# Kernel tuning notes

Hardware: AMD Instinct MI355X
Metric: run time of the kernel (lower is better)

## Reference

```python
import jax, jax.numpy as jnp
import numpy as np

N = 50000
E = 800000
F_IN = 128
HEADS = 4
OUT_PER_HEAD = 32  # out_features 128 / 4 heads
NEG_SLOPE = 0.2


def setup_inputs() -> dict:
    key = jax.random.key(0)
    k1, k2, k3, k4, k5 = jax.random.split(key, 5)
    x = jax.random.normal(k1, (N, F_IN), dtype=jnp.float32)
    edge_index = jax.random.randint(k2, (2, E), 0, N, dtype=jnp.int64)
    # xavier-uniform style init
    limW = float(np.sqrt(6.0 / (F_IN + OUT_PER_HEAD)))
    W = jax.random.uniform(k3, (HEADS, F_IN, OUT_PER_HEAD), jnp.float32, -limW, limW)
    lima = float(np.sqrt(6.0 / (OUT_PER_HEAD + 1)))
    a_l = jax.random.uniform(k4, (HEADS, OUT_PER_HEAD), jnp.float32, -lima, lima)
    a_r = jax.random.uniform(k5, (HEADS, OUT_PER_HEAD), jnp.float32, -lima, lima)
    return {"x": x, "edge_index": edge_index, "W": W, "a_l": a_l, "a_r": a_r}


def _leaky_relu(v, slope):
    return jnp.where(v >= 0, v, slope * v)


def reference(x, edge_index, W, a_l, a_r):
    src, dst = edge_index[0], edge_index[1]
    n = x.shape[0]
    # Wh: [heads, N, out_per_head]
    Wh = jnp.einsum('nf,kfh->knh', x, W)
    e_l = jnp.einsum('knh,kh->kn', Wh, a_l)  # [heads, N]
    e_r = jnp.einsum('knh,kh->kn', Wh, a_r)
    # per-edge attention logits [heads, E]
    e = _leaky_relu(e_l[:, src] + e_r[:, dst], NEG_SLOPE)
    # segment softmax over incoming edges of each dst node
    seg_max = jax.vmap(lambda ee: jax.ops.segment_max(ee, dst, num_segments=n))(e)
    seg_max = jnp.maximum(seg_max, -1e9)  # torch init value for empty nodes
    exp_e = jnp.exp(e - seg_max[:, dst])
    denom = jax.vmap(lambda ee: jax.ops.segment_sum(ee, dst, num_segments=n))(exp_e)
    alpha = exp_e / (denom[:, dst] + 1e-16)  # [heads, E]
    # weighted aggregation: [heads, E, out_per_head] scattered into [heads, N, out_per_head]
    weighted = alpha[..., None] * Wh[:, src, :]
    out = jax.vmap(lambda w: jax.ops.segment_sum(w, dst, num_segments=n))(weighted)
    # concat heads -> [N, heads*out_per_head]
    return out.transpose(1, 0, 2).reshape(n, -1)
```

## Files before the change

kernel.cpp:

```cpp
#include <hip/hip_runtime.h>

#define NN 50000
#define NE 800000
#define FIN 128
#define NH 4
#define OPH 32
#define FOUT 128
#define NSLOPE 0.2f
#define NGB ((NN + 63) / 64)
#define BCOLS 144
#define LDA 136
#define BSH 5
#define BUKSZ 32
#define NBUK ((NN + BUKSZ - 1) >> BSH)
#define SUBCH 4096
#define NPSUB ((NE + SUBCH - 1) / SUBCH)
#define NSC ((NPSUB + 3) / 4)
#define SLOTQ 15
#define SLOTS 64
#define GRID1 (NPSUB + NGB)

typedef __attribute__((ext_vector_type(8))) short short8v;
typedef __attribute__((ext_vector_type(4))) float f32x4;

static __device__ __forceinline__ unsigned short f2bf(float f) {
  unsigned int u = __float_as_uint(f);
  u += 0x7fffu + ((u >> 16) & 1u);
  return (unsigned short)(u >> 16);
}

__global__ __launch_bounds__(128) void k_prep(
    const float* __restrict__ W, const float* __restrict__ a_l,
    const float* __restrict__ a_r, unsigned short* __restrict__ Btf) {
  const int c = blockIdx.x;
  const int f = threadIdx.x;
  unsigned short v = 0;
  if (c < 128) {
    const int h = c >> 5, o = c & 31;
    v = f2bf(W[h * (FIN * OPH) + f * OPH + o]);
  } else if (c < 136) {
    const int j = c - 128;
    const int h = j & 3;
    const float* __restrict__ av = (j < 4) ? a_l : a_r;
    float s = 0.f;
    for (int o = 0; o < 32; ++o)
      s += W[h * (FIN * OPH) + f * OPH + o] * av[h * OPH + o];
    v = f2bf(s);
  }
  const int ct = c >> 4, lr = c & 15;
  const int s = f >> 5, rem = f & 31, lk = rem >> 3, j = rem & 7;
  const int l = lr + 16 * lk;
  Btf[(((size_t)ct * 4 + s) * 64 + l) * 8 + j] = v;
}

__global__ __launch_bounds__(256) void k_gemm_part(
    const float* __restrict__ x, const unsigned short* __restrict__ Btf,
    const int* __restrict__ src, const int* __restrict__ dst,
    unsigned int* __restrict__ ebuf,
    unsigned short* __restrict__ WhU, float* __restrict__ e_l4,
    float* __restrict__ e_r4) {
  __shared__ union U {
    unsigned short As[64 * LDA];
    int cntl[NBUK];
  } sh;
  const int t = threadIdx.x;
  const int bid = blockIdx.x;

  if (bid < NPSUB) {
    const int pidx = bid;
    const int sc = pidx >> 2;
    const int sub = pidx & 3;
    const int base = pidx * SUBCH;
    for (int b = t; b < NBUK; b += 256) sh.cntl[b] = 0;
    __syncthreads();
    unsigned int* __restrict__ myreg =
        ebuf + (size_t)sc * NBUK * 64 + sub * 16;
#pragma unroll
    for (int k = 0; k < SUBCH / 256; ++k) {
      const int i = base + k * 256 + t;
      if (i < NE) {
        const int d = dst[i];
        const int b = d >> BSH;
        const int lp = atomicAdd(&sh.cntl[b], 1);
        if (lp < SLOTQ)
          myreg[(size_t)b * 64 + 1 + lp] =
              ((unsigned int)(d & (BUKSZ - 1)) << 16) | (unsigned int)src[i];
      }
    }
    __syncthreads();
    for (int b = t; b < NBUK; b += 256)
      myreg[(size_t)b * 64] = (unsigned int)min(sh.cntl[b], SLOTQ);
    return;
  }

  const int g = bid - NPSUB;
  if (g >= NGB) return;
  const int m0 = g * 64;

#pragma unroll
  for (int i = 0; i < 8; ++i) {
    const int fidx = t + i * 256;
    const int node = fidx >> 5;
    const int fg = fidx & 31;
    const int n = m0 + node;
    float4 v = make_float4(0.f, 0.f, 0.f, 0.f);
    if (n < NN) v = *(const float4*)(x + (size_t)n * FIN + fg * 4);
    ushort4 pk;
    pk.x = f2bf(v.x); pk.y = f2bf(v.y); pk.z = f2bf(v.z); pk.w = f2bf(v.w);
    *(ushort4*)&sh.As[node * LDA + fg * 4] = pk;
  }
  __syncthreads();

  const int w = t >> 6;
  const int l = t & 63;
  const int lr = l & 15;
  const int lk = l >> 4;

  short8v a_frag[4];
#pragma unroll
  for (int kk = 0; kk < 4; ++kk)
    a_frag[kk] = *(const short8v*)&sh.As[(w * 16 + lr) * LDA + kk * 32 + lk * 8];

  f32x4 acc[9];
#pragma unroll
  for (int ct = 0; ct < 9; ++ct) acc[ct] = (f32x4){0.f, 0.f, 0.f, 0.f};

#pragma unroll
  for (int ct = 0; ct < 9; ++ct) {
    const unsigned short* __restrict__ Bp = Btf + ((size_t)ct * 4) * 512 + l * 8;
    short8v b0 = *(const short8v*)(Bp);
    short8v b1 = *(const short8v*)(Bp + 512);
    short8v b2 = *(const short8v*)(Bp + 1024);
    short8v b3 = *(const short8v*)(Bp + 1536);
    acc[ct] = __builtin_amdgcn_mfma_f32_16x16x32_bf16(a_frag[0], b0, acc[ct], 0, 0, 0);
    acc[ct] = __builtin_amdgcn_mfma_f32_16x16x32_bf16(a_frag[1], b1, acc[ct], 0, 0, 0);
    acc[ct] = __builtin_amdgcn_mfma_f32_16x16x32_bf16(a_frag[2], b2, acc[ct], 0, 0, 0);
    acc[ct] = __builtin_amdgcn_mfma_f32_16x16x32_bf16(a_frag[3], b3, acc[ct], 0, 0, 0);
  }

#pragma unroll
  for (int ct = 0; ct < 9; ++ct) {
#pragma unroll
    for (int reg = 0; reg < 4; ++reg) {
      const int n = m0 + w * 16 + lk * 4 + reg;
      if (n >= NN) continue;
      const float v = acc[ct][reg];
      if (ct < 8) {
        WhU[(size_t)n * FOUT + ct * 16 + lr] = f2bf(v);
      } else if (lr < 4) {
        e_l4[n * NH + lr] = v;
      } else if (lr < 8) {
        e_r4[n * NH + (lr - 4)] = v;
      }
    }
  }
}

__global__ __launch_bounds__(256) void k_lists(
    const unsigned int* __restrict__ ebuf,
    unsigned short* __restrict__ lists_g, int* __restrict__ degs) {
  __shared__ __align__(16) unsigned short lists[BUKSZ][SLOTS];
  __shared__ int cur[BUKSZ];

  const int b = blockIdx.x;
  const int t = threadIdx.x;
  const int w = t >> 6;
  const int lane = t & 63;

  if (t < BUKSZ) cur[t] = 0;
  __syncthreads();

  const int word = lane & 15;
#pragma unroll
  for (int it = 0; it < (NPSUB + 15) / 16; ++it) {
    const int j = it * 16 + w * 4 + (lane >> 4);
    unsigned int v = 0;
    if (j < NPSUB) {
      const int sc = j >> 2, sub = j & 3;
      v = ebuf[(size_t)sc * NBUK * 64 + (size_t)b * 64 + sub * 16 + word];
    }
    const unsigned int cnt = __shfl(v, lane & 48);
    if (j < NPSUB && word >= 1 && word <= (int)cnt) {
      const int idx = (int)(v >> 16);
      const int lp = atomicAdd(&cur[idx], 1);
      if (lp < SLOTS) lists[idx][lp] = (unsigned short)(v & 0xFFFFu);
    }
  }
  __syncthreads();

  const int idx = t >> 3, ch = t & 7;
  const int node = b * BUKSZ + idx;
  if (node < NN) {
    const uint4 pk = *(const uint4*)&lists[idx][ch * 8];
    *(uint4*)&lists_g[(size_t)node * SLOTS + ch * 8] = pk;
  }
  if (t < BUKSZ && b * BUKSZ + t < NN)
    degs[b * BUKSZ + t] = min(cur[t], SLOTS);
}

__global__ __launch_bounds__(256) void k_agg(
    const int* __restrict__ degs, const unsigned short* __restrict__ lists_g,
    const float* __restrict__ e_l4, const float* __restrict__ e_r4,
    const unsigned int* __restrict__ Whh, float* __restrict__ out) {
  __shared__ unsigned short ls[4][64];
  __shared__ float exs[4][64][4];

  const int t = threadIdx.x;
  const int w = t >> 6;
  const int lane = t & 63;
  const int n = blockIdx.x * 4 + w;

  const int deg = min(degs[n], SLOTS);
  const float4 ern = *(const float4*)&e_r4[n * NH];
  const unsigned short s16 = lists_g[(size_t)n * SLOTS + lane];
  ls[w][lane] = s16;

  float e0 = 0.f, e1 = 0.f, e2 = 0.f, e3 = 0.f;
  if (lane < deg) {
    const int s = (int)s16;
    const float4 el = *(const float4*)&e_l4[s * NH];
    float l0 = el.x + ern.x; l0 = (l0 >= 0.f) ? l0 : NSLOPE * l0;
    float l1 = el.y + ern.y; l1 = (l1 >= 0.f) ? l1 : NSLOPE * l1;
    float l2 = el.z + ern.z; l2 = (l2 >= 0.f) ? l2 : NSLOPE * l2;
    float l3 = el.w + ern.w; l3 = (l3 >= 0.f) ? l3 : NSLOPE * l3;
    e0 = __expf(l0); e1 = __expf(l1);
    e2 = __expf(l2); e3 = __expf(l3);
  }
  *(float4*)exs[w][lane] = make_float4(e0, e1, e2, e3);

  const int h = lane >> 4;
  float acc0 = 0.f, acc1 = 0.f, den = 0.f;
  int jl = 0;
  for (; jl + 7 < deg; jl += 8) {
    int sj[8];
#pragma unroll
    for (int u = 0; u < 8; ++u) sj[u] = ls[w][jl + u];
    unsigned int vv[8];
#pragma unroll
    for (int u = 0; u < 8; ++u) vv[u] = Whh[(size_t)sj[u] * 64 + lane];
#pragma unroll
    for (int u = 0; u < 8; ++u) {
      const float wH = exs[w][jl + u][h];
      den += wH;
      acc0 = fmaf(wH, __uint_as_float(vv[u] << 16), acc0);
      acc1 = fmaf(wH, __uint_as_float(vv[u] & 0xffff0000u), acc1);
    }
  }
  for (; jl < deg; ++jl) {
    const int sj = ls[w][jl];
    const float wH = exs[w][jl][h];
    const unsigned int v = Whh[(size_t)sj * 64 + lane];
    den += wH;
    acc0 = fmaf(wH, __uint_as_float(v << 16), acc0);
    acc1 = fmaf(wH, __uint_as_float(v & 0xffff0000u), acc1);
  }

  const float inv = 1.f / (den + 1e-16f);
  *(float2*)&out[(size_t)n * FOUT + 2 * lane] =
      make_float2(acc0 * inv, acc1 * inv);
}

extern "C" void kernel_launch(void* const* d_in, const int* in_sizes, int n_in,
                              void* d_out, int out_size, void* d_ws, size_t ws_size,
                              hipStream_t stream) {
  const float* x   = (const float*)d_in[0];
  const int*   ei  = (const int*)d_in[1];
  const float* W   = (const float*)d_in[2];
  const float* a_l = (const float*)d_in[3];
  const float* a_r = (const float*)d_in[4];
  float* out = (float*)d_out;

  const int* src = ei;
  const int* dst = ei + NE;

  unsigned int* Whh = (unsigned int*)d_ws;
  float* e_l4     = (float*)(Whh + (size_t)NN * 64);
  float* e_r4     = e_l4 + NN * NH;
  unsigned short* Btf = (unsigned short*)(e_r4 + NN * NH);
  unsigned int* ebuf = (unsigned int*)(Btf + 9 * 4 * 64 * 8);
  unsigned short* lists_g = (unsigned short*)(ebuf + (size_t)NSC * NBUK * 64);
  int* degs = (int*)(lists_g + (size_t)NN * SLOTS);
  (void)ws_size; (void)in_sizes; (void)n_in; (void)out_size;

  k_prep<<<BCOLS, 128, 0, stream>>>(W, a_l, a_r, Btf);

  k_gemm_part<<<GRID1, 256, 0, stream>>>(
      x, Btf, src, dst, ebuf, (unsigned short*)Whh, e_l4, e_r4);

  k_lists<<<NBUK, 256, 0, stream>>>(ebuf, lists_g, degs);

  k_agg<<<NN / 4, 256, 0, stream>>>(degs, lists_g, e_l4, e_r4, Whh, out);
}
```

Measured before the change: 70.28 us.

## Split Wh into per-head planes and aggregate one head per block

The GEMM now writes Wh as four head-major bf16 planes of shape [N,32] instead of one interleaved [N,128] row. The aggregation kernel launches one block per (head, 4-node group) and swizzles block IDs so neighbouring blocks share a head, which shrinks each gather's working set to one head's plane and is meant to improve L2 reuse. Each wave splits the edges across two half-waves, gathering 2-byte values per lane, and combines the halves with a shuffle. The cost is four times as many blocks, redundant reads of degrees and lists per head, and narrower 16-bit gathers. The lists kernel also zero-fills its shared slots so unused entries no longer hold stale data.

```diff
diff --git a/kernel.cpp b/kernel.cpp
--- a/kernel.cpp
+++ b/kernel.cpp
@@ -57,7 +57,7 @@
     const float* __restrict__ x, const unsigned short* __restrict__ Btf,
     const int* __restrict__ src, const int* __restrict__ dst,
     unsigned int* __restrict__ ebuf,
-    unsigned short* __restrict__ WhU, float* __restrict__ e_l4,
+    unsigned short* __restrict__ WhhH, float* __restrict__ e_l4,
     float* __restrict__ e_r4) {
   __shared__ union U {
     unsigned short As[64 * LDA];
@@ -146,7 +146,8 @@
       if (n >= NN) continue;
       const float v = acc[ct][reg];
       if (ct < 8) {
-        WhU[(size_t)n * FOUT + ct * 16 + lr] = f2bf(v);
+        const int h2 = ct >> 1;
+        WhhH[((size_t)h2 * NN + n) * 32 + (ct & 1) * 16 + lr] = f2bf(v);
       } else if (lr < 4) {
         e_l4[n * NH + lr] = v;
       } else if (lr < 8) {
@@ -168,6 +169,11 @@
   const int lane = t & 63;
 
   if (t < BUKSZ) cur[t] = 0;
+  {
+    const int idx0 = t >> 3, ch0 = t & 7;
+    uint4 z; z.x = z.y = z.z = z.w = 0u;
+    *(uint4*)&lists[idx0][ch0 * 8] = z;
+  }
   __syncthreads();
 
   const int word = lane & 15;
@@ -201,63 +207,70 @@
 __global__ __launch_bounds__(256) void k_agg(
     const int* __restrict__ degs, const unsigned short* __restrict__ lists_g,
     const float* __restrict__ e_l4, const float* __restrict__ e_r4,
-    const unsigned int* __restrict__ Whh, float* __restrict__ out) {
+    const unsigned short* __restrict__ WhhH, float* __restrict__ out) {
   __shared__ unsigned short ls[4][64];
-  __shared__ float exs[4][64][4];
+  __shared__ float exs[4][64];
 
   const int t = threadIdx.x;
   const int w = t >> 6;
   const int lane = t & 63;
-  const int n = blockIdx.x * 4 + w;
+  const int bid = blockIdx.x;
+
+  const int h = (bid & 7) >> 1;
+  const int ng = (bid >> 3) * 2 + (bid & 1);
+  const int n = ng * 4 + w;
 
   const int deg = min(degs[n], SLOTS);
-  const float4 ern = *(const float4*)&e_r4[n * NH];
+  const float ern = e_r4[n * NH + h];
   const unsigned short s16 = lists_g[(size_t)n * SLOTS + lane];
-  ls[w][lane] = s16;
-
-  float e0 = 0.f, e1 = 0.f, e2 = 0.f, e3 = 0.f;
+  ls[w][lane] = (lane < deg) ? s16 : (unsigned short)0;
+
+  float e = 0.f;
   if (lane < deg) {
-    const int s = (int)s16;
-    const float4 el = *(const float4*)&e_l4[s * NH];
-    float l0 = el.x + ern.x; l0 = (l0 >= 0.f) ? l0 : NSLOPE * l0;
-    float l1 = el.y + ern.y; l1 = (l1 >= 0.f) ? l1 : NSLOPE * l1;
-    float l2 = el.z + ern.z; l2 = (l2 >= 0.f) ? l2 : NSLOPE * l2;
-    float l3 = el.w + ern.w; l3 = (l3 >= 0.f) ? l3 : NSLOPE * l3;
-    e0 = __expf(l0); e1 = __expf(l1);
-    e2 = __expf(l2); e3 = __expf(l3);
-  }
-  *(float4*)exs[w][lane] = make_float4(e0, e1, e2, e3);
-
-  const int h = lane >> 4;
-  float acc0 = 0.f, acc1 = 0.f, den = 0.f;
+    float l = e_l4[(int)s16 * NH + h] + ern;
+    l = (l >= 0.f) ? l : NSLOPE * l;
+    e = __expf(l);
+  }
+  exs[w][lane] = e;
+
+  const int col = lane & 31;
+  const int eh = lane >> 5;
+  const unsigned short* __restrict__ T = WhhH + (size_t)h * NN * 32;
+
+  float acc = 0.f, den = 0.f;
   int jl = 0;
   for (; jl + 7 < deg; jl += 8) {
-    int sj[8];
-#pragma unroll
-    for (int u = 0; u < 8; ++u) sj[u] = ls[w][jl + u];
-    unsigned int vv[8];
-#pragma unroll
-    for (int u = 0; u < 8; ++u) vv[u] = Whh[(size_t)sj[u] * 64 + lane];
-#pragma unroll
-    for (int u = 0; u < 8; ++u) {
-      const float wH = exs[w][jl + u][h];
-      den += wH;
-      acc0 = fmaf(wH, __uint_as_float(vv[u] << 16), acc0);
-      acc1 = fmaf(wH, __uint_as_float(vv[u] & 0xffff0000u), acc1);
-    }
-  }
-  for (; jl < deg; ++jl) {
-    const int sj = ls[w][jl];
-    const float wH = exs[w][jl][h];
-    const unsigned int v = Whh[(size_t)sj * 64 + lane];
+    int sj[4]; float wv[4];
+#pragma unroll
+    for (int u = 0; u < 4; ++u) {
+      const int e2 = jl + u * 2 + eh;
+      sj[u] = ls[w][e2];
+      wv[u] = exs[w][e2];
+    }
+    unsigned short vv[4];
+#pragma unroll
+    for (int u = 0; u < 4; ++u) vv[u] = T[(size_t)sj[u] * 32 + col];
+#pragma unroll
+    for (int u = 0; u < 4; ++u) {
+      den += wv[u];
+      acc = fmaf(wv[u], __uint_as_float((unsigned int)vv[u] << 16), acc);
+    }
+  }
+  for (; jl < deg; jl += 2) {
+    const int e2 = jl + eh;
+    const int sj = ls[w][e2];
+    const float wH = exs[w][e2];
+    const unsigned short v = T[(size_t)sj * 32 + col];
     den += wH;
-    acc0 = fmaf(wH, __uint_as_float(v << 16), acc0);
-    acc1 = fmaf(wH, __uint_as_float(v & 0xffff0000u), acc1);
-  }
-
-  const float inv = 1.f / (den + 1e-16f);
-  *(float2*)&out[(size_t)n * FOUT + 2 * lane] =
-      make_float2(acc0 * inv, acc1 * inv);
+    acc = fmaf(wH, __uint_as_float((unsigned int)v << 16), acc);
+  }
+
+  acc += __shfl_xor(acc, 32);
+  den += __shfl_xor(den, 32);
+
+  if (lane < 32) {
+    out[(size_t)n * FOUT + h * OPH + col] = acc / (den + 1e-16f);
+  }
 }
 
 extern "C" void kernel_launch(void* const* d_in, const int* in_sizes, int n_in,
@@ -273,8 +286,8 @@
   const int* src = ei;
   const int* dst = ei + NE;
 
-  unsigned int* Whh = (unsigned int*)d_ws;
-  float* e_l4     = (float*)(Whh + (size_t)NN * 64);
+  unsigned short* WhhH = (unsigned short*)d_ws;
+  float* e_l4     = (float*)(WhhH + (size_t)NH * NN * 32);
   float* e_r4     = e_l4 + NN * NH;
   unsigned short* Btf = (unsigned short*)(e_r4 + NN * NH);
   unsigned int* ebuf = (unsigned int*)(Btf + 9 * 4 * 64 * 8);
@@ -285,9 +298,9 @@
   k_prep<<<BCOLS, 128, 0, stream>>>(W, a_l, a_r, Btf);
 
   k_gemm_part<<<GRID1, 256, 0, stream>>>(
-      x, Btf, src, dst, ebuf, (unsigned short*)Whh, e_l4, e_r4);
+      x, Btf, src, dst, ebuf, WhhH, e_l4, e_r4);
 
   k_lists<<<NBUK, 256, 0, stream>>>(ebuf, lists_g, degs);
 
-  k_agg<<<NN / 4, 256, 0, stream>>>(degs, lists_g, e_l4, e_r4, Whh, out);
-}
+  k_agg<<<NN, 256, 0, stream>>>(degs, lists_g, e_l4, e_r4, WhhH, out);
+}
```

Measured after the change: 105.2 us. 49.6% more time.
